# Performance work log

Measured on AMD Instinct MI355X. Metric: run time of the kernel, lower is better.

The kernel has to match this reference:

```python
import jax, jax.numpy as jnp
import numpy as np
from jax.ops import segment_sum, segment_max

H, D, HID, L, B = 4, 32, 128, 2, 64  # heads, head_dim, hidden, layers, graphs
NB, NS, NC, NF = 100000, 20000, 10000, 2000


def setup_inputs() -> dict:
    key = jax.random.key(0)
    ks = iter(jax.random.split(key, 64))
    nrm = lambda shape, s=1.0: jax.random.normal(next(ks), shape, jnp.float32) * s
    ridx = lambda n, hi: jax.random.randint(next(ks), (n,), 0, hi, jnp.int32)
    srt = lambda n, hi: jnp.sort(jax.random.randint(next(ks), (n,), 0, hi, jnp.int32))
    return {
        'x_block': nrm((NB, 8)), 'x_spmt': nrm((NS, 10)),
        'x_crane': nrm((NC, 7)), 'x_facility': nrm((NF, 3)),
        'Wp_b': nrm((8, HID), 0.2), 'bp_b': jnp.zeros((HID,), jnp.float32),
        'Wp_s': nrm((10, HID), 0.2), 'bp_s': jnp.zeros((HID,), jnp.float32),
        'Wp_c': nrm((7, HID), 0.2), 'bp_c': jnp.zeros((HID,), jnp.float32),
        'Wp_f': nrm((3, HID), 0.2), 'bp_f': jnp.zeros((HID,), jnp.float32),
        'gat_W': nrm((L, 8, HID, HID), 0.05),
        'gat_as': nrm((L, 8, H, D), 0.1), 'gat_ad': nrm((L, 8, H, D), 0.1),
        'gat_b': jnp.zeros((L, 8, HID), jnp.float32),
        'ln_s': jnp.ones((L, HID), jnp.float32), 'ln_b': jnp.zeros((L, HID), jnp.float32),
        'e_nt_s': ridx(800000, NB), 'e_nt_d': ridx(800000, NS),
        'e_ct_s': ridx(800000, NS), 'e_ct_d': ridx(800000, NB),
        'e_nl_s': ridx(400000, NB), 'e_nl_d': ridx(400000, NC),
        'e_cl_s': ridx(400000, NC), 'e_cl_d': ridx(400000, NB),
        'e_ba_s': ridx(100000, NB), 'e_ba_d': ridx(100000, NF),
        'e_pr_s': ridx(800000, NB), 'e_pr_d': ridx(800000, NB),
        'e_sa_s': ridx(20000, NS), 'e_sa_d': ridx(20000, NF),
        'e_ca_s': ridx(10000, NC), 'e_ca_d': ridx(10000, NF),
        'b_block': srt(NB, B), 'b_spmt': srt(NS, B),
        'b_crane': srt(NC, B), 'b_facility': srt(NF, B),
    }


def layer_norm(x, s, b):
    mu = x.mean(-1, keepdims=True)
    v = ((x - mu) ** 2).mean(-1, keepdims=True)
    return (x - mu) / jnp.sqrt(v + 1e-5) * s + b


def gat(h_src, h_dst, src, dst, W, a_s, a_d, bias):
    # PyG GATConv (shared lin for src/dst, add_self_loops=False, eval mode)
    n_dst = h_dst.shape[0]
    hs = (h_src @ W).reshape(-1, H, D)                 # [Ns,H,D]
    hd = (h_dst @ W).reshape(-1, H, D)                 # [Nd,H,D]
    al_s = (hs * a_s).sum(-1)                          # [Ns,H]
    al_d = (hd * a_d).sum(-1)                          # [Nd,H]
    e = jax.nn.leaky_relu(al_s[src] + al_d[dst], 0.2)  # [E,H]
    m = segment_max(e, dst, num_segments=n_dst)
    m = jnp.where(jnp.isfinite(m), m, 0.0)             # empty segments
    ex = jnp.exp(e - m[dst])
    den = segment_sum(ex, dst, num_segments=n_dst)
    coef = ex / (den[dst] + 1e-16)                     # scatter-softmax
    msg = hs[src] * coef[..., None]                    # [E,H,D]
    out = segment_sum(msg, dst, num_segments=n_dst)
    return out.reshape(n_dst, H * D) + bias


def pool(x, b):
    s = segment_sum(x, b, num_segments=B)
    c = segment_sum(jnp.ones((x.shape[0],), x.dtype), b, num_segments=B)
    return s / jnp.clip(c, 1.0)[:, None]


def reference(x_block, x_spmt, x_crane, x_facility,
              Wp_b, bp_b, Wp_s, bp_s, Wp_c, bp_c, Wp_f, bp_f,
              gat_W, gat_as, gat_ad, gat_b, ln_s, ln_b,
              e_nt_s, e_nt_d, e_ct_s, e_ct_d, e_nl_s, e_nl_d, e_cl_s, e_cl_d,
              e_ba_s, e_ba_d, e_pr_s, e_pr_d, e_sa_s, e_sa_d, e_ca_s, e_ca_d,
              b_block, b_spmt, b_crane, b_facility):
    xb = x_block @ Wp_b + bp_b
    xs = x_spmt @ Wp_s + bp_s
    xc = x_crane @ Wp_c + bp_c
    xf = x_facility @ Wp_f + bp_f
    rels = [(0, 'b', 's', e_nt_s, e_nt_d), (1, 's', 'b', e_ct_s, e_ct_d),
            (2, 'b', 'c', e_nl_s, e_nl_d), (3, 'c', 'b', e_cl_s, e_cl_d),
            (4, 'b', 'f', e_ba_s, e_ba_d), (5, 'b', 'b', e_pr_s, e_pr_d),
            (6, 's', 'f', e_sa_s, e_sa_d), (7, 'c', 'f', e_ca_s, e_ca_d)]
    for l in range(L):
        x = {'b': xb, 's': xs, 'c': xc, 'f': xf}
        acc = {k: [] for k in x}
        for r, st, dt, src, dst in rels:
            acc[dt].append(gat(x[st], x[dt], src, dst,
                               gat_W[l, r], gat_as[l, r], gat_ad[l, r], gat_b[l, r]))
        new = {k: sum(v) / len(v) for k, v in acc.items()}  # HeteroConv mean
        xb = layer_norm(jax.nn.relu(new['b']) + xb, ln_s[l], ln_b[l])
        xs = layer_norm(jax.nn.relu(new['s']) + xs, ln_s[l], ln_b[l])
        xc = layer_norm(jax.nn.relu(new['c']) + xc, ln_s[l], ln_b[l])
        xf = layer_norm(jax.nn.relu(new['f']) + xf, ln_s[l], ln_b[l])
    return jnp.concatenate([pool(xb, b_block), pool(xs, b_spmt),
                            pool(xc, b_crane), pool(xf, b_facility)], axis=-1)
```

## Files before the change

kernel.cpp:

```cpp
#include <hip/hip_runtime.h>
#include <hip/hip_bf16.h>
#include <cstdint>

#define HID 128
#define NHEAD 4
#define NGRAPH 64
#define PCHUNK 32

typedef __attribute__((ext_vector_type(8))) short bf16x8;
typedef __attribute__((ext_vector_type(4))) short bf16x4s;
typedef __attribute__((ext_vector_type(4))) float f32x4;

__device__ __forceinline__ float bf2f(short u) {
    union { float f; unsigned int i; } c;
    c.i = ((unsigned int)(unsigned short)u) << 16;
    return c.f;
}
__device__ __forceinline__ float lrelu(float a) { return (a > 0.f) ? a : 0.2f * a; }

struct PrePack {
    const int* edst[8]; int* deg[8]; int E[8]; int h_off[9];
    const float* px[4]; const float* pW[4]; const float* pb[4]; float* po[4];
    int pN[4]; int pK[4]; int p_off[5];
    const float* gat_W; __hip_bfloat16* Wsw;
    const float* gat_as; const float* gat_ad; float* vecall;
};

__global__ __launch_bounds__(256) void k_pre(PrePack A) {
    int b = blockIdx.x;
    int tid = threadIdx.x;
    if (b < A.h_off[8]) {
#pragma unroll
        for (int r = 0; r < 8; ++r) {
            if (b >= A.h_off[r] && b < A.h_off[r + 1]) {
                int e = (b - A.h_off[r]) * 256 + tid;
                if (e < A.E[r]) atomicAdd(&A.deg[r][A.edst[r][e]], 1);
            }
        }
        return;
    }
    b -= A.h_off[8];
    if (b < A.p_off[4]) {
#pragma unroll
        for (int t = 0; t < 4; ++t) {
            if (b >= A.p_off[t] && b < A.p_off[t + 1]) {
                int idx = (b - A.p_off[t]) * 256 + tid;
                if (idx < A.pN[t] * HID) {
                    int row = idx >> 7, c = idx & 127;
                    int K = A.pK[t];
                    float acc = A.pb[t][c];
                    for (int k = 0; k < K; ++k) acc += A.px[t][row * K + k] * A.pW[t][k * HID + c];
                    A.po[t][idx] = acc;
                }
            }
        }
        return;
    }
    b -= A.p_off[4];
    if (b < 1024) {
        int idx = b * 256 + tid;
        int l = idx >> 17;
        int rem = idx & 131071;
        int k = rem >> 10;
        int gc = rem & 1023;
        int rel, n, gobase, Ncols;
        if (gc < 512) {
            int i = gc >> 7;
            rel = (i == 0) ? 0 : (i == 1) ? 2 : (i == 2) ? 4 : 5;
            n = gc; gobase = 0; Ncols = 512;
        } else if (gc < 768) {
            int c2 = gc - 512;
            rel = (c2 >> 7) ? 6 : 1;
            n = c2; gobase = 65536; Ncols = 256;
        } else {
            int c2 = gc - 768;
            rel = (c2 >> 7) ? 7 : 3;
            n = c2; gobase = 98304; Ncols = 256;
        }
        int nl = n & 127;
        float v = A.gat_W[(((size_t)l * 8 + rel) * 128 + k) * 128 + nl];
        size_t dst = (size_t)l * 131072 + gobase + ((size_t)(k >> 3) * Ncols + n) * 8 + (k & 7);
        A.Wsw[dst] = __float2bfloat16(v);
        return;
    }
    b -= 1024;
    {
        int idx = b * 256 + tid;
        if (idx < 16384) {
            int h = idx & 3, k = (idx >> 2) & 127, p = (idx >> 9) & 15, l = idx >> 13;
            int r = p >> 1, side = p & 1;
            const float* W = A.gat_W + (((size_t)l * 8 + r) * 128 + k) * 128;
            const float* a = (side ? A.gat_ad : A.gat_as) + ((size_t)l * 8 + r) * 128;
            float s = 0.f;
#pragma unroll
            for (int j = 0; j < 32; ++j) s += W[h * 32 + j] * a[h * 32 + j];
            A.vecall[((size_t)l * 16 + p) * 512 + k * 4 + h] = s;
        }
    }
}

struct CsrPack {
    const int* esrc[8];
    const int* edst[8];
    int* deg[8];
    int* offs[8];
    int* curs[8];
    int* adj[8];
    int E[8];
    int Nd[8];
};

__global__ void k_scan_part_all(CsrPack P, int* __restrict__ part_all) {
    int r = blockIdx.y;
    int N = P.Nd[r];
    if (blockIdx.x * 256 >= N) return;
    __shared__ int sh[256];
    int t = threadIdx.x, i = blockIdx.x * 256 + t;
    sh[t] = (i < N) ? P.deg[r][i] : 0;
    __syncthreads();
    for (int o = 128; o; o >>= 1) {
        if (t < o) sh[t] += sh[t + o];
        __syncthreads();
    }
    if (t == 0) part_all[r * 512 + blockIdx.x] = sh[0];
}
__global__ void k_scan_top_all(int* __restrict__ part_all, CsrPack P) {
    int r = blockIdx.x;
    int n = (P.Nd[r] + 255) / 256;
    __shared__ int sh[512];
    int t = threadIdx.x;
    int v = (t < n) ? part_all[r * 512 + t] : 0;
    sh[t] = v;
    __syncthreads();
    for (int o = 1; o < 512; o <<= 1) {
        int tmp = (t >= o) ? sh[t - o] : 0;
        __syncthreads();
        sh[t] += tmp;
        __syncthreads();
    }
    if (t < n) part_all[r * 512 + t] = sh[t] - v;
}
__global__ void k_scan_down_all(CsrPack P, const int* __restrict__ part_all) {
    int r = blockIdx.y;
    int N = P.Nd[r];
    if (blockIdx.x * 256 >= N) return;
    __shared__ int sh[256];
    int t = threadIdx.x, i = blockIdx.x * 256 + t;
    int v = (i < N) ? P.deg[r][i] : 0;
    sh[t] = v;
    __syncthreads();
    for (int o = 1; o < 256; o <<= 1) {
        int tmp = (t >= o) ? sh[t - o] : 0;
        __syncthreads();
        sh[t] += tmp;
        __syncthreads();
    }
    if (i < N) {
        int excl = sh[t] - v + part_all[r * 512 + blockIdx.x];
        P.offs[r][i] = excl;
        P.curs[r][i] = excl;
    }
}

__device__ __forceinline__ void gemm_body(char* smemraw, const float* __restrict__ A,
                                          const __hip_bfloat16* __restrict__ Bsw,
                                          __hip_bfloat16* __restrict__ out,
                                          int M, int Ncols, int bx, int by) {
    __hip_bfloat16 (*Alds)[136] = (__hip_bfloat16 (*)[136])smemraw;
    int m0 = bx * 64, n0 = by * 128;
    int t = threadIdx.x;
    for (int i = t; i < 2048; i += 256) {
        int row = i >> 5, ch = i & 31;
        float4 v = make_float4(0.f, 0.f, 0.f, 0.f);
        if (m0 + row < M) v = *(const float4*)(A + (size_t)(m0 + row) * 128 + ch * 4);
        __hip_bfloat16* dp = &Alds[row][ch * 4];
        dp[0] = __float2bfloat16(v.x);
        dp[1] = __float2bfloat16(v.y);
        dp[2] = __float2bfloat16(v.z);
        dp[3] = __float2bfloat16(v.w);
    }
    __syncthreads();
    int w = t >> 6, l = t & 63;
    int lane16 = l & 15, q = l >> 4;
    f32x4 acc[8];
#pragma unroll
    for (int nn = 0; nn < 8; ++nn) acc[nn] = (f32x4){0.f, 0.f, 0.f, 0.f};
    const __hip_bfloat16* arow = &Alds[w * 16 + lane16][q * 8];
#pragma unroll
    for (int kk = 0; kk < 4; ++kk) {
        bf16x8 a = *(const bf16x8*)(arow + kk * 32);
#pragma unroll
        for (int nn = 0; nn < 8; ++nn) {
            size_t boff = ((size_t)(kk * 4 + q) * Ncols + (n0 + nn * 16 + lane16)) * 8;
            bf16x8 b = *(const bf16x8*)(Bsw + boff);
            acc[nn] = __builtin_amdgcn_mfma_f32_16x16x32_bf16(a, b, acc[nn], 0, 0, 0);
        }
    }
    int orow = m0 + w * 16 + q * 4;
#pragma unroll
    for (int nn = 0; nn < 8; ++nn) {
        int col = n0 + nn * 16 + lane16;
#pragma unroll
        for (int r = 0; r < 4; ++r) {
            int row = orow + r;
            if (row < M) out[(size_t)row * Ncols + col] = __float2bfloat16(acc[nn][r]);
        }
    }
}

__device__ __forceinline__ void logits_body(char* smemraw,
                                            const float* const vec[7], float* const outp[7],
                                            const float* __restrict__ x, int N, int nv, int bloc) {
    float (*vs)[128][4] = (float (*)[128][4])smemraw;
    int t = threadIdx.x;
    for (int i = t; i < nv * 512; i += 256) {
        int v = i >> 9, j = i & 511;
        vs[v][j >> 2][j & 3] = vec[v][j];
    }
    __syncthreads();
    int nl = t >> 2, h = t & 3;
    int node = bloc * 64 + nl;
    if (node >= N) return;
    const float* xr = x + (size_t)node * 128;
    float acc[7];
#pragma unroll
    for (int v = 0; v < 7; ++v) acc[v] = 0.f;
#pragma unroll 4
    for (int k = 0; k < 128; ++k) {
        float xv = xr[k];
#pragma unroll
        for (int v = 0; v < 7; ++v)
            if (v < nv) acc[v] += xv * vs[v][k][h];
    }
#pragma unroll
    for (int v = 0; v < 7; ++v)
        if (v < nv) outp[v][node * 4 + h] = acc[v];
}

struct MidPack {
    const int* esrc[8]; const int* edst[8]; int* curs[8]; int* adj[8];
    int E[8]; int sc_off[9];
    const float* gA[3]; const __hip_bfloat16* gB[3]; __hip_bfloat16* gO[3];
    int gM[3]; int gNc[3]; int gMB[3]; int g_off[4];
    const float* lvec[4][7]; float* lout[4][7]; const float* lx[4];
    int lN[4]; int lnv[4]; int l_off[5];
};

__global__ __launch_bounds__(256) void k_mid(MidPack M) {
    __shared__ __align__(16) char smem[17408];
    int b = blockIdx.x;
    if (b < M.sc_off[8]) {
#pragma unroll
        for (int r = 0; r < 8; ++r) {
            if (b >= M.sc_off[r] && b < M.sc_off[r + 1]) {
                int e = (b - M.sc_off[r]) * 256 + threadIdx.x;
                if (e < M.E[r]) {
                    int slot = atomicAdd(&M.curs[r][M.edst[r][e]], 1);
                    M.adj[r][slot] = M.esrc[r][e];
                }
            }
        }
        return;
    }
    b -= M.sc_off[8];
    if (b < M.g_off[3]) {
#pragma unroll
        for (int g = 0; g < 3; ++g) {
            if (b >= M.g_off[g] && b < M.g_off[g + 1]) {
                int local = b - M.g_off[g];
                int bx = local % M.gMB[g];
                int by = local / M.gMB[g];
                gemm_body(smem, M.gA[g], M.gB[g], M.gO[g], M.gM[g], M.gNc[g], bx, by);
            }
        }
        return;
    }
    b -= M.g_off[3];
#pragma unroll
    for (int t = 0; t < 4; ++t) {
        if (b >= M.l_off[t] && b < M.l_off[t + 1]) {
            logits_body(smem, M.lvec[t], M.lout[t], M.lx[t], M.lN[t], M.lnv[t], b - M.l_off[t]);
        }
    }
}

struct RelArg {
    const __hip_bfloat16* hs;
    int hstride;
    int hoff;
    const float* als;
    const float* ald;
    const int* adj;
    const int* off;
    const int* deg;
    const float* bias;
};

__device__ __forceinline__ void dst_body(const RelArg& r0, const RelArg& r1, const RelArg& r2,
                                         int nrel, float inv_nrel, float* __restrict__ x,
                                         const float* __restrict__ ln_s,
                                         const float* __restrict__ ln_b, int N, int bloc) {
    int wv = threadIdx.x >> 6, lane = threadIdx.x & 63;
    int half = lane >> 5, sl = lane & 31;
    int d = bloc * 8 + wv * 2 + half;
    if (d >= N) return;
    int c0 = sl * 4;
    int h = sl >> 3;
    float4 xv = *(const float4*)&x[(size_t)d * HID + c0];
    float rel0 = 0.f, rel1 = 0.f, rel2 = 0.f, rel3 = 0.f;
    for (int rr = 0; rr < nrel; ++rr) {
        const RelArg& R = (rr == 0) ? r0 : (rr == 1) ? r1 : r2;
        int base = R.off[d];
        int dg = R.deg[d];
        float aldh = R.ald[d * NHEAD + h];
        const __hip_bfloat16* hp = R.hs + R.hoff + c0;
        const int hstr = R.hstride;
        const int* ap = R.adj + base;
        const float* als = R.als;
        float a0 = 0.f, a1 = 0.f, a2 = 0.f, a3 = 0.f, den = 0.f;
        int k = 0;
        for (; k + 4 <= dg; k += 4) {
            int s0 = ap[k], s1 = ap[k + 1], s2 = ap[k + 2], s3 = ap[k + 3];
            float w0 = __expf(lrelu(als[s0 * NHEAD + h] + aldh));
            float w1 = __expf(lrelu(als[s1 * NHEAD + h] + aldh));
            float w2 = __expf(lrelu(als[s2 * NHEAD + h] + aldh));
            float w3 = __expf(lrelu(als[s3 * NHEAD + h] + aldh));
            bf16x4s v0 = *(const bf16x4s*)(hp + (size_t)s0 * hstr);
            bf16x4s v1 = *(const bf16x4s*)(hp + (size_t)s1 * hstr);
            bf16x4s v2 = *(const bf16x4s*)(hp + (size_t)s2 * hstr);
            bf16x4s v3 = *(const bf16x4s*)(hp + (size_t)s3 * hstr);
            a0 += w0 * bf2f(v0[0]) + w1 * bf2f(v1[0]) + w2 * bf2f(v2[0]) + w3 * bf2f(v3[0]);
            a1 += w0 * bf2f(v0[1]) + w1 * bf2f(v1[1]) + w2 * bf2f(v2[1]) + w3 * bf2f(v3[1]);
            a2 += w0 * bf2f(v0[2]) + w1 * bf2f(v1[2]) + w2 * bf2f(v2[2]) + w3 * bf2f(v3[2]);
            a3 += w0 * bf2f(v0[3]) + w1 * bf2f(v1[3]) + w2 * bf2f(v2[3]) + w3 * bf2f(v3[3]);
            den += w0 + w1 + w2 + w3;
        }
        for (; k < dg; ++k) {
            int s = ap[k];
            float w = __expf(lrelu(als[s * NHEAD + h] + aldh));
            bf16x4s v = *(const bf16x4s*)(hp + (size_t)s * hstr);
            a0 += w * bf2f(v[0]);
            a1 += w * bf2f(v[1]);
            a2 += w * bf2f(v[2]);
            a3 += w * bf2f(v[3]);
            den += w;
        }
        float inv = 1.f / (den + 1e-16f);
        rel0 += a0 * inv + R.bias[c0];
        rel1 += a1 * inv + R.bias[c0 + 1];
        rel2 += a2 * inv + R.bias[c0 + 2];
        rel3 += a3 * inv + R.bias[c0 + 3];
    }
    float v0 = rel0 * inv_nrel, v1 = rel1 * inv_nrel;
    float v2 = rel2 * inv_nrel, v3 = rel3 * inv_nrel;
    v0 = (v0 > 0.f) ? v0 : 0.f;
    v1 = (v1 > 0.f) ? v1 : 0.f;
    v2 = (v2 > 0.f) ? v2 : 0.f;
    v3 = (v3 > 0.f) ? v3 : 0.f;
    v0 += xv.x; v1 += xv.y; v2 += xv.z; v3 += xv.w;
    float s = v0 + v1 + v2 + v3;
    float ss = v0 * v0 + v1 * v1 + v2 * v2 + v3 * v3;
#pragma unroll
    for (int o = 16; o; o >>= 1) {
        s += __shfl_xor(s, o);
        ss += __shfl_xor(ss, o);
    }
    float mu = s * (1.f / HID);
    float var = ss * (1.f / HID) - mu * mu;
    float rstd = rsqrtf(var + 1e-5f);
    float o0 = (v0 - mu) * rstd * ln_s[c0] + ln_b[c0];
    float o1 = (v1 - mu) * rstd * ln_s[c0 + 1] + ln_b[c0 + 1];
    float o2 = (v2 - mu) * rstd * ln_s[c0 + 2] + ln_b[c0 + 2];
    float o3 = (v3 - mu) * rstd * ln_s[c0 + 3] + ln_b[c0 + 3];
    *(float4*)&x[(size_t)d * HID + c0] = make_float4(o0, o1, o2, o3);
}

struct TypeArg {
    RelArg r0, r1, r2;
    float* x;
    int N;
    int nrel;
    float inv_nrel;
};

__global__ __launch_bounds__(256) void k_dst_all(TypeArg t0, TypeArg t1, TypeArg t2, TypeArg t3,
                                                 int off1, int off2, int off3,
                                                 const float* __restrict__ ln_s,
                                                 const float* __restrict__ ln_b) {
    int b = blockIdx.x;
    if (b < off1) {
        dst_body(t0.r0, t0.r1, t0.r2, t0.nrel, t0.inv_nrel, t0.x, ln_s, ln_b, t0.N, b);
    } else if (b < off2) {
        dst_body(t1.r0, t1.r1, t1.r2, t1.nrel, t1.inv_nrel, t1.x, ln_s, ln_b, t1.N, b - off1);
    } else if (b < off3) {
        dst_body(t2.r0, t2.r1, t2.r2, t2.nrel, t2.inv_nrel, t2.x, ln_s, ln_b, t2.N, b - off2);
    } else {
        dst_body(t3.r0, t3.r1, t3.r2, t3.nrel, t3.inv_nrel, t3.x, ln_s, ln_b, t3.N, b - off3);
    }
}

__global__ void k_pool_all(const float* __restrict__ x0, const float* __restrict__ x1,
                           const float* __restrict__ x2, const float* __restrict__ x3,
                           const int* __restrict__ b0, const int* __restrict__ b1,
                           const int* __restrict__ b2, const int* __restrict__ b3,
                           int N0, int N1, int N2, int N3, float* __restrict__ out) {
    int ty = blockIdx.y;
    const float* x;
    const int* b;
    int N, toff;
    if (ty == 0)      { x = x0; b = b0; N = N0; toff = 0; }
    else if (ty == 1) { x = x1; b = b1; N = N1; toff = 128; }
    else if (ty == 2) { x = x2; b = b2; N = N2; toff = 256; }
    else              { x = x3; b = b3; N = N3; toff = 384; }
    int r0 = blockIdx.x * PCHUNK;
    if (r0 >= N) return;
    int rend = min(r0 + PCHUNK, N);
    int c = threadIdx.x;
    int cur = b[r0];
    float acc = 0.f;
    for (int i = r0; i < rend; ++i) {
        int g = b[i];
        if (g != cur) {
            atomicAdd(&out[cur * 512 + toff + c], acc);
            acc = 0.f;
            cur = g;
        }
        acc += x[(size_t)i * HID + c];
    }
    atomicAdd(&out[cur * 512 + toff + c], acc);
}
__global__ void k_cnt(const int* __restrict__ b0, const int* __restrict__ b1,
                      const int* __restrict__ b2, const int* __restrict__ b3,
                      int N0, int N1, int N2, int N3, float* __restrict__ cnt) {
    int i = blockIdx.x * blockDim.x + threadIdx.x;
    if (i >= 256) return;
    int t = i >> 6, g = i & 63;
    const int* b = (t == 0) ? b0 : (t == 1) ? b1 : (t == 2) ? b2 : b3;
    int N = (t == 0) ? N0 : (t == 1) ? N1 : (t == 2) ? N2 : N3;
    int lo = 0, hi = N;
    while (lo < hi) { int m = (lo + hi) >> 1; if (b[m] < g) lo = m + 1; else hi = m; }
    int s = lo;
    hi = N;
    while (lo < hi) { int m = (lo + hi) >> 1; if (b[m] < g + 1) lo = m + 1; else hi = m; }
    cnt[i] = (float)(lo - s);
}
__global__ void k_div(float* __restrict__ out, const float* __restrict__ cnt) {
    int idx = blockIdx.x * blockDim.x + threadIdx.x;
    if (idx >= NGRAPH * 512) return;
    int g = idx >> 9, c = idx & 511, t = c >> 7;
    out[idx] = out[idx] / fmaxf(cnt[t * NGRAPH + g], 1.0f);
}

extern "C" void kernel_launch(void* const* d_in, const int* in_sizes, int n_in,
                              void* d_out, int out_size, void* d_ws, size_t ws_size,
                              hipStream_t stream) {
    const float* x_in[4] = {(const float*)d_in[0], (const float*)d_in[1],
                            (const float*)d_in[2], (const float*)d_in[3]};
    const float* Wp[4] = {(const float*)d_in[4], (const float*)d_in[6],
                          (const float*)d_in[8], (const float*)d_in[10]};
    const float* bp[4] = {(const float*)d_in[5], (const float*)d_in[7],
                          (const float*)d_in[9], (const float*)d_in[11]};
    const float* gat_W  = (const float*)d_in[12];
    const float* gat_as = (const float*)d_in[13];
    const float* gat_ad = (const float*)d_in[14];
    const float* gat_b  = (const float*)d_in[15];
    const float* ln_s   = (const float*)d_in[16];
    const float* ln_b   = (const float*)d_in[17];
    const int* esrc[8] = {(const int*)d_in[18], (const int*)d_in[20], (const int*)d_in[22],
                          (const int*)d_in[24], (const int*)d_in[26], (const int*)d_in[28],
                          (const int*)d_in[30], (const int*)d_in[32]};
    const int* edst[8] = {(const int*)d_in[19], (const int*)d_in[21], (const int*)d_in[23],
                          (const int*)d_in[25], (const int*)d_in[27], (const int*)d_in[29],
                          (const int*)d_in[31], (const int*)d_in[33]};
    const int* bidx[4] = {(const int*)d_in[34], (const int*)d_in[35],
                          (const int*)d_in[36], (const int*)d_in[37]};
    int E[8];
    {
        const int eidx[8] = {18, 20, 22, 24, 26, 28, 30, 32};
        for (int r = 0; r < 8; ++r) E[r] = in_sizes[eidx[r]];
    }
    const int Kin[4] = {8, 10, 7, 3};
    int N[4];
    for (int t = 0; t < 4; ++t) N[t] = in_sizes[t] / Kin[t];
    const int rel_st[8] = {0, 1, 0, 2, 0, 0, 1, 2};
    const int rel_dt[8] = {1, 0, 2, 0, 3, 0, 3, 3};
    const int rel_hoff[8] = {0, 0, 128, 0, 256, 384, 128, 128};
    const int grp_stride[4] = {512, 256, 256, 0};
    (void)ws_size; (void)n_in;

    char* wbase = (char*)d_ws;
    size_t cur = 0;
    auto alloc = [&](size_t bytes) -> void* {
        void* p = wbase + cur;
        cur += (bytes + 15) & ~(size_t)15;
        return p;
    };
    float* x[4];
    for (int t = 0; t < 4; ++t) x[t] = (float*)alloc((size_t)N[t] * HID * 4);
    __hip_bfloat16* hs_g[3];
    hs_g[0] = (__hip_bfloat16*)alloc((size_t)N[0] * 512 * 2);
    hs_g[1] = (__hip_bfloat16*)alloc((size_t)N[1] * 256 * 2);
    hs_g[2] = (__hip_bfloat16*)alloc((size_t)N[2] * 256 * 2);
    __hip_bfloat16* Wsw = (__hip_bfloat16*)alloc((size_t)2 * 131072 * 2);
    float* vecall = (float*)alloc((size_t)2 * 16 * 512 * 4);
    float *als_[8], *ald_[8];
    int *deg[8], *offs[8], *curs[8], *adj[8];
    int NdTot = 0;
    for (int r = 0; r < 8; ++r) NdTot += N[rel_dt[r]] + 4;
    int* deg_all = (int*)alloc((size_t)NdTot * 4);
    {
        int off = 0;
        for (int r = 0; r < 8; ++r) { deg[r] = deg_all + off; off += N[rel_dt[r]] + 4; }
    }
    for (int r = 0; r < 8; ++r) {
        int Ns = N[rel_st[r]], Nd = N[rel_dt[r]];
        als_[r] = (float*)alloc((size_t)Ns * NHEAD * 4);
        ald_[r] = (float*)alloc((size_t)Nd * NHEAD * 4);
        offs[r] = (int*)alloc((size_t)Nd * 4);
        curs[r] = (int*)alloc((size_t)Nd * 4);
        adj[r]  = (int*)alloc((size_t)E[r] * 4);
    }
    int* part_all = (int*)alloc(8 * 512 * 4);
    float* cntf   = (float*)alloc(256 * 4);

    CsrPack CP;
    int NdMax = 0;
    for (int r = 0; r < 8; ++r) {
        CP.esrc[r] = esrc[r]; CP.edst[r] = edst[r];
        CP.deg[r] = deg[r]; CP.offs[r] = offs[r]; CP.curs[r] = curs[r]; CP.adj[r] = adj[r];
        CP.E[r] = E[r]; CP.Nd[r] = N[rel_dt[r]];
        if (CP.Nd[r] > NdMax) NdMax = CP.Nd[r];
    }

    hipMemsetAsync(deg_all, 0, (size_t)NdTot * 4, stream);
    PrePack PA;
    {
        for (int r = 0; r < 8; ++r) { PA.edst[r] = edst[r]; PA.deg[r] = deg[r]; PA.E[r] = E[r]; }
        PA.h_off[0] = 0;
        for (int r = 0; r < 8; ++r) PA.h_off[r + 1] = PA.h_off[r] + (E[r] + 255) / 256;
        for (int t = 0; t < 4; ++t) {
            PA.px[t] = x_in[t]; PA.pW[t] = Wp[t]; PA.pb[t] = bp[t]; PA.po[t] = x[t];
            PA.pN[t] = N[t]; PA.pK[t] = Kin[t];
        }
        PA.p_off[0] = 0;
        for (int t = 0; t < 4; ++t) PA.p_off[t + 1] = PA.p_off[t] + (N[t] * HID + 255) / 256;
        PA.gat_W = gat_W; PA.Wsw = Wsw;
        PA.gat_as = gat_as; PA.gat_ad = gat_ad; PA.vecall = vecall;
        int total = PA.h_off[8] + PA.p_off[4] + 1024 + 64;
        k_pre<<<total, 256, 0, stream>>>(PA);
    }

    {
        dim3 gn((NdMax + 255) / 256, 8);
        k_scan_part_all<<<gn, 256, 0, stream>>>(CP, part_all);
        k_scan_top_all<<<8, 512, 0, stream>>>(part_all, CP);
        k_scan_down_all<<<gn, 256, 0, stream>>>(CP, part_all);
    }

    const size_t g_woff[3] = {0, 65536, 98304};
    const int g_ncols[3] = {512, 256, 256};
    int nb[4];
    for (int t = 0; t < 4; ++t) nb[t] = (N[t] + 7) / 8;
    int doff1 = nb[0], doff2 = nb[0] + nb[1], doff3 = nb[0] + nb[1] + nb[2];
    int dtot = doff3 + nb[3];

    for (int l = 0; l < 2; ++l) {
        MidPack M;
        if (l == 0) {
            for (int r = 0; r < 8; ++r) {
                M.esrc[r] = esrc[r]; M.edst[r] = edst[r];
                M.curs[r] = curs[r]; M.adj[r] = adj[r]; M.E[r] = E[r];
            }
            M.sc_off[0] = 0;
            for (int r = 0; r < 8; ++r) M.sc_off[r + 1] = M.sc_off[r] + (E[r] + 255) / 256;
        } else {
            for (int r = 0; r < 8; ++r) {
                M.esrc[r] = esrc[r]; M.edst[r] = edst[r];
                M.curs[r] = curs[r]; M.adj[r] = adj[r]; M.E[r] = E[r];
            }
            for (int r = 0; r <= 8; ++r) M.sc_off[r] = 0;
        }
        M.g_off[0] = 0;
        for (int g = 0; g < 3; ++g) {
            M.gA[g] = x[g];
            M.gB[g] = Wsw + (size_t)l * 131072 + g_woff[g];
            M.gO[g] = hs_g[g];
            M.gM[g] = N[g];
            M.gNc[g] = g_ncols[g];
            M.gMB[g] = (N[g] + 63) / 64;
            M.g_off[g + 1] = M.g_off[g] + M.gMB[g] * (g_ncols[g] / 128);
        }
        const float* vl = vecall + (size_t)l * 16 * 512;
        auto vvec = [&](int r, int side) { return vl + (size_t)(r * 2 + side) * 512; };
        for (int t = 0; t < 4; ++t)
            for (int v = 0; v < 7; ++v) { M.lvec[t][v] = vl; M.lout[t][v] = als_[0]; }
        M.lvec[0][0] = vvec(0, 0); M.lout[0][0] = als_[0];
        M.lvec[0][1] = vvec(2, 0); M.lout[0][1] = als_[2];
        M.lvec[0][2] = vvec(4, 0); M.lout[0][2] = als_[4];
        M.lvec[0][3] = vvec(5, 0); M.lout[0][3] = als_[5];
        M.lvec[0][4] = vvec(1, 1); M.lout[0][4] = ald_[1];
        M.lvec[0][5] = vvec(3, 1); M.lout[0][5] = ald_[3];
        M.lvec[0][6] = vvec(5, 1); M.lout[0][6] = ald_[5];
        M.lvec[1][0] = vvec(1, 0); M.lout[1][0] = als_[1];
        M.lvec[1][1] = vvec(6, 0); M.lout[1][1] = als_[6];
        M.lvec[1][2] = vvec(0, 1); M.lout[1][2] = ald_[0];
        M.lvec[2][0] = vvec(3, 0); M.lout[2][0] = als_[3];
        M.lvec[2][1] = vvec(7, 0); M.lout[2][1] = als_[7];
        M.lvec[2][2] = vvec(2, 1); M.lout[2][2] = ald_[2];
        M.lvec[3][0] = vvec(4, 1); M.lout[3][0] = ald_[4];
        M.lvec[3][1] = vvec(6, 1); M.lout[3][1] = ald_[6];
        M.lvec[3][2] = vvec(7, 1); M.lout[3][2] = ald_[7];
        const int lnv[4] = {7, 3, 3, 3};
        M.l_off[0] = 0;
        for (int t = 0; t < 4; ++t) {
            M.lx[t] = x[t]; M.lN[t] = N[t]; M.lnv[t] = lnv[t];
            M.l_off[t + 1] = M.l_off[t] + (N[t] + 63) / 64;
        }
        int total = M.sc_off[8] + M.g_off[3] + M.l_off[4];
        k_mid<<<total, 256, 0, stream>>>(M);

        auto mk = [&](int r) {
            RelArg a;
            int st = rel_st[r];
            a.hs = hs_g[st]; a.hstride = grp_stride[st]; a.hoff = rel_hoff[r];
            a.als = als_[r]; a.ald = ald_[r];
            a.adj = adj[r]; a.off = offs[r]; a.deg = deg[r];
            a.bias = gat_b + (size_t)(l * 8 + r) * HID;
            return a;
        };
        TypeArg T[4];
        const int trels[4][3] = {{1, 3, 5}, {0, 0, 0}, {2, 2, 2}, {4, 6, 7}};
        const int tnrel[4] = {3, 1, 1, 3};
        const float tinv[4] = {1.f / 3.f, 1.f, 1.f, 1.f / 3.f};
        for (int t = 0; t < 4; ++t) {
            T[t].r0 = mk(trels[t][0]);
            T[t].r1 = mk(trels[t][1]);
            T[t].r2 = mk(trels[t][2]);
            T[t].x = x[t];
            T[t].N = N[t];
            T[t].nrel = tnrel[t];
            T[t].inv_nrel = tinv[t];
        }
        k_dst_all<<<dtot, 256, 0, stream>>>(T[0], T[1], T[2], T[3], doff1, doff2, doff3,
                                            ln_s + l * HID, ln_b + l * HID);
    }

    hipMemsetAsync(d_out, 0, (size_t)out_size * 4, stream);
    k_cnt<<<1, 256, 0, stream>>>(bidx[0], bidx[1], bidx[2], bidx[3],
                                 N[0], N[1], N[2], N[3], cntf);
    {
        int pmax = 0;
        for (int t = 0; t < 4; ++t) {
            int p = (N[t] + PCHUNK - 1) / PCHUNK;
            if (p > pmax) pmax = p;
        }
        dim3 gp(pmax, 4);
        k_pool_all<<<gp, 128, 0, stream>>>(x[0], x[1], x[2], x[3],
                                           bidx[0], bidx[1], bidx[2], bidx[3],
                                           N[0], N[1], N[2], N[3], (float*)d_out);
    }
    k_div<<<(NGRAPH * 512 + 255) / 256, 256, 0, stream>>>((float*)d_out, cntf);
}
```

Before: 1.340 ms.

## Bin edges by destination range before CSR scatter to localize atomics

The CSR fill scatter is pulled out of the fused mid kernel and replaced by a two-pass binning scheme. Edges are first partitioned into 8 destination-range bins in a staging buffer, then a second pass does the cursor atomics and adjacency writes bin by bin. The aim is to confine the random atomic and scatter traffic to a smaller address window at a time, for better cache locality. It costs an extra read and write of every edge through the staging buffer, plus extra kernel launches, and the scatter no longer overlaps with the layer-0 GEMM and logits work.

```diff
diff --git a/kernel.cpp b/kernel.cpp
--- a/kernel.cpp
+++ b/kernel.cpp
@@ -162,6 +162,80 @@
     }
 }
 
+struct BinPack {
+    const int* esrc[8]; const int* edst[8];
+    uint2* staging[8];
+    int* curs[8]; int* adj[8];
+    int* binCnt; int* binBase; int* binCur;
+    int E[8]; int Nd[8]; int binshift[8];
+};
+
+__global__ void k_binscan(BinPack B, const int* __restrict__ part_all) {
+    int r = threadIdx.x;
+    if (r >= 8) return;
+    int cnt[8];
+#pragma unroll
+    for (int b = 0; b < 8; ++b) cnt[b] = 0;
+    int nparts = (B.Nd[r] + 255) >> 8;
+    int cshift = B.binshift[r] - 8;
+    for (int c = 0; c < nparts; ++c) cnt[c >> cshift] += part_all[r * 512 + c];
+    int run = 0;
+    for (int b = 0; b < 8; ++b) {
+        B.binCnt[r * 8 + b] = cnt[b];
+        B.binBase[r * 8 + b] = run;
+        B.binCur[r * 8 + b] = run;
+        run += cnt[b];
+    }
+}
+
+__global__ __launch_bounds__(256) void k_binp1(BinPack B) {
+    int r = blockIdx.y;
+    int E = B.E[r];
+    int sh = B.binshift[r];
+    __shared__ int h[8], base[8], rk[8];
+    int tid = threadIdx.x;
+    for (int e0 = blockIdx.x * 256; e0 < E; e0 += gridDim.x * 256) {
+        if (tid < 8) { h[tid] = 0; rk[tid] = 0; }
+        __syncthreads();
+        int e = e0 + tid;
+        int valid = e < E;
+        int src = 0, dst = 0, bin = 0;
+        if (valid) {
+            src = B.esrc[r][e];
+            dst = B.edst[r][e];
+            bin = dst >> sh;
+            atomicAdd(&h[bin], 1);
+        }
+        __syncthreads();
+        if (tid < 8 && h[tid] > 0) base[tid] = atomicAdd(&B.binCur[r * 8 + tid], h[tid]);
+        __syncthreads();
+        if (valid) {
+            int pos = base[bin] + atomicAdd(&rk[bin], 1);
+            B.staging[r][pos] = make_uint2((unsigned)src, (unsigned)dst);
+        }
+        __syncthreads();
+    }
+}
+
+__global__ __launch_bounds__(256) void k_binp2(BinPack B) {
+    int r = blockIdx.y;
+    int bin = blockIdx.x & 7;
+    int cstart = blockIdx.x >> 3;
+    int nstride = gridDim.x >> 3;
+    int cnt = B.binCnt[r * 8 + bin];
+    const uint2* st = B.staging[r] + B.binBase[r * 8 + bin];
+    int* curs = B.curs[r];
+    int* adj = B.adj[r];
+    for (int i0 = cstart * 256; i0 < cnt; i0 += nstride * 256) {
+        int i = i0 + threadIdx.x;
+        if (i < cnt) {
+            uint2 ed = st[i];
+            int slot = atomicAdd(&curs[ed.y], 1);
+            adj[slot] = (int)ed.x;
+        }
+    }
+}
+
 __device__ __forceinline__ void gemm_body(char* smemraw, const float* __restrict__ A,
                                           const __hip_bfloat16* __restrict__ Bsw,
                                           __hip_bfloat16* __restrict__ out,
@@ -238,8 +312,6 @@
 }
 
 struct MidPack {
-    const int* esrc[8]; const int* edst[8]; int* curs[8]; int* adj[8];
-    int E[8]; int sc_off[9];
     const float* gA[3]; const __hip_bfloat16* gB[3]; __hip_bfloat16* gO[3];
     int gM[3]; int gNc[3]; int gMB[3]; int g_off[4];
     const float* lvec[4][7]; float* lout[4][7]; const float* lx[4];
@@ -249,20 +321,6 @@
 __global__ __launch_bounds__(256) void k_mid(MidPack M) {
     __shared__ __align__(16) char smem[17408];
     int b = blockIdx.x;
-    if (b < M.sc_off[8]) {
-#pragma unroll
-        for (int r = 0; r < 8; ++r) {
-            if (b >= M.sc_off[r] && b < M.sc_off[r + 1]) {
-                int e = (b - M.sc_off[r]) * 256 + threadIdx.x;
-                if (e < M.E[r]) {
-                    int slot = atomicAdd(&M.curs[r][M.edst[r][e]], 1);
-                    M.adj[r][slot] = M.esrc[r][e];
-                }
-            }
-        }
-        return;
-    }
-    b -= M.sc_off[8];
     if (b < M.g_off[3]) {
 #pragma unroll
         for (int g = 0; g < 3; ++g) {
@@ -505,6 +563,7 @@
     float* vecall = (float*)alloc((size_t)2 * 16 * 512 * 4);
     float *als_[8], *ald_[8];
     int *deg[8], *offs[8], *curs[8], *adj[8];
+    uint2* staging[8];
     int NdTot = 0;
     for (int r = 0; r < 8; ++r) NdTot += N[rel_dt[r]] + 4;
     int* deg_all = (int*)alloc((size_t)NdTot * 4);
@@ -519,18 +578,34 @@
         offs[r] = (int*)alloc((size_t)Nd * 4);
         curs[r] = (int*)alloc((size_t)Nd * 4);
         adj[r]  = (int*)alloc((size_t)E[r] * 4);
+        staging[r] = (uint2*)alloc((size_t)E[r] * 8);
     }
     int* part_all = (int*)alloc(8 * 512 * 4);
+    int* binCnt   = (int*)alloc(64 * 4);
+    int* binBase  = (int*)alloc(64 * 4);
+    int* binCur   = (int*)alloc(64 * 4);
     float* cntf   = (float*)alloc(256 * 4);
 
     CsrPack CP;
-    int NdMax = 0;
+    int NdMax = 0, Emax = 0;
     for (int r = 0; r < 8; ++r) {
         CP.esrc[r] = esrc[r]; CP.edst[r] = edst[r];
         CP.deg[r] = deg[r]; CP.offs[r] = offs[r]; CP.curs[r] = curs[r]; CP.adj[r] = adj[r];
         CP.E[r] = E[r]; CP.Nd[r] = N[rel_dt[r]];
         if (CP.Nd[r] > NdMax) NdMax = CP.Nd[r];
-    }
+        if (E[r] > Emax) Emax = E[r];
+    }
+    BinPack BP;
+    for (int r = 0; r < 8; ++r) {
+        BP.esrc[r] = esrc[r]; BP.edst[r] = edst[r];
+        BP.staging[r] = staging[r];
+        BP.curs[r] = curs[r]; BP.adj[r] = adj[r];
+        BP.E[r] = E[r]; BP.Nd[r] = N[rel_dt[r]];
+        int sh = 8;
+        while (((BP.Nd[r] - 1) >> sh) > 7) ++sh;
+        BP.binshift[r] = sh;
+    }
+    BP.binCnt = binCnt; BP.binBase = binBase; BP.binCur = binCur;
 
     hipMemsetAsync(deg_all, 0, (size_t)NdTot * 4, stream);
     PrePack PA;
@@ -553,9 +628,18 @@
     {
         dim3 gn((NdMax + 255) / 256, 8);
         k_scan_part_all<<<gn, 256, 0, stream>>>(CP, part_all);
+        k_binscan<<<1, 64, 0, stream>>>(BP, part_all);
         k_scan_top_all<<<8, 512, 0, stream>>>(part_all, CP);
         k_scan_down_all<<<gn, 256, 0, stream>>>(CP, part_all);
-    }
+        dim3 g1(512, 8);
+        k_binp1<<<g1, 256, 0, stream>>>(BP);
+        dim3 g2(512, 8);
+        k_binp2<<<g2, 256, 0, stream>>>(BP);
+    }
+
+    hipMemsetAsync(d_out, 0, (size_t)out_size * 4, stream);
+    k_cnt<<<1, 256, 0, stream>>>(bidx[0], bidx[1], bidx[2], bidx[3],
+                                 N[0], N[1], N[2], N[3], cntf);
 
     const size_t g_woff[3] = {0, 65536, 98304};
     const int g_ncols[3] = {512, 256, 256};
@@ -566,20 +650,6 @@
 
     for (int l = 0; l < 2; ++l) {
         MidPack M;
-        if (l == 0) {
-            for (int r = 0; r < 8; ++r) {
-                M.esrc[r] = esrc[r]; M.edst[r] = edst[r];
-                M.curs[r] = curs[r]; M.adj[r] = adj[r]; M.E[r] = E[r];
-            }
-            M.sc_off[0] = 0;
-            for (int r = 0; r < 8; ++r) M.sc_off[r + 1] = M.sc_off[r] + (E[r] + 255) / 256;
-        } else {
-            for (int r = 0; r < 8; ++r) {
-                M.esrc[r] = esrc[r]; M.edst[r] = edst[r];
-                M.curs[r] = curs[r]; M.adj[r] = adj[r]; M.E[r] = E[r];
-            }
-            for (int r = 0; r <= 8; ++r) M.sc_off[r] = 0;
-        }
         M.g_off[0] = 0;
         for (int g = 0; g < 3; ++g) {
             M.gA[g] = x[g];
@@ -616,7 +686,7 @@
             M.lx[t] = x[t]; M.lN[t] = N[t]; M.lnv[t] = lnv[t];
             M.l_off[t + 1] = M.l_off[t] + (N[t] + 63) / 64;
         }
-        int total = M.sc_off[8] + M.g_off[3] + M.l_off[4];
+        int total = M.g_off[3] + M.l_off[4];
         k_mid<<<total, 256, 0, stream>>>(M);
 
         auto mk = [&](int r) {
@@ -645,9 +715,6 @@
                                             ln_s + l * HID, ln_b + l * HID);
     }
 
-    hipMemsetAsync(d_out, 0, (size_t)out_size * 4, stream);
-    k_cnt<<<1, 256, 0, stream>>>(bidx[0], bidx[1], bidx[2], bidx[3],
-                                 N[0], N[1], N[2], N[3], cntf);
     {
         int pmax = 0;
         for (int t = 0; t < 4; ++t) {
```

Result: slower. 1.384 ms (+3.3%).
